# Performance work log

Hardware: AMD Instinct MI355X
Metric: run time of the kernel (lower is better)

Reference implementation:

```python
import jax, jax.numpy as jnp
import numpy as np
from jax import lax

V, H, A, S = 256, 2048, 512, 512  # vocab, hidden, attn, seq_len


def setup_inputs() -> dict:
    key = jax.random.key(0)
    ks = jax.random.split(key, 8)
    sc = 0.02  # small init to keep tanh unsaturated
    return {
        "x_enc": jax.random.normal(ks[0], (S, V), jnp.float32),
        "x_dec": jax.random.normal(ks[1], (S, V), jnp.float32),
        "W_enc": jax.random.normal(ks[2], (H, V + H), jnp.float32) * sc,
        "b_enc": jnp.zeros((H,), jnp.float32),
        "Wa_enc": jax.random.normal(ks[3], (A, H), jnp.float32) * sc,
        "Wa_dec": jax.random.normal(ks[4], (A, H), jnp.float32) * sc,
        "v_a": jax.random.normal(ks[5], (A,), jnp.float32) * sc,
        "W_dec": jax.random.normal(ks[6], (H, V + 2 * H), jnp.float32) * sc,
        "b_dec": jnp.zeros((H,), jnp.float32),
        "W_out": jax.random.normal(ks[7], (V, H), jnp.float32) * sc,
        "b_out": jnp.zeros((V,), jnp.float32),
    }


def reference(x_enc, x_dec, W_enc, b_enc, Wa_enc, Wa_dec, v_a, W_dec, b_dec, W_out, b_out):
    h0 = jnp.zeros((W_enc.shape[0],), x_enc.dtype)

    # Encoder: h_t = tanh(W_enc [x_t ; h_{t-1}] + b)
    def enc_step(h, x):
        h_new = jnp.tanh(jnp.concatenate([x, h]) @ W_enc.T + b_enc)
        return h_new, h_new

    h_enc, enc_states = lax.scan(enc_step, h0, x_enc)  # enc_states: (S, H)

    # Encoder-side attention projection is step-invariant -> hoist (same math).
    enc_proj = enc_states @ Wa_enc.T  # (S, A)

    # Decoder with per-step Bahdanau additive attention.
    def dec_step(h, x):
        dec_proj = h @ Wa_dec.T                              # (A,)
        energy = jnp.tanh(enc_proj + dec_proj) @ v_a         # (S,)
        attn_w = jax.nn.softmax(energy)                      # (S,)
        context = attn_w @ enc_states                        # (H,)
        h_new = jnp.tanh(jnp.concatenate([x, context, h]) @ W_dec.T + b_dec)
        logits = h_new @ W_out.T + b_out                     # (V,)
        return h_new, logits

    _, outputs = lax.scan(dec_step, h_enc, x_dec)  # (S, V)
    return outputs
```

## Files before the change

### kernel.cpp

```cpp
#include <hip/hip_runtime.h>

#define V 256
#define H 2048
#define A 512
#define S 512
#define NBLK 128
#define NTHR 512
#define CH 64

typedef float f32x4 __attribute__((ext_vector_type(4)));

__device__ __forceinline__ void st_chunk(float* p, float x, float y, int tag) {
    f32x4 v; v.x = x; v.y = y; v.z = 0.f; v.w = __int_as_float(tag);
    asm volatile("global_store_dwordx4 %0, %1, off sc0 sc1" :: "v"(p), "v"(v) : "memory");
}
__device__ __forceinline__ f32x4 poll1(const float* p, int tag) {
    f32x4 r;
    for (;;) {
        asm volatile("global_load_dwordx4 %0, %1, off sc0 sc1\n\ts_waitcnt vmcnt(0)"
                     : "=&v"(r) : "v"(p) : "memory");
        if (__float_as_int(r.w) == tag) return r;
    }
}
__device__ __forceinline__ void poll2(const float* p0, const float* p1, int tag,
                                      f32x4& a, f32x4& b) {
    for (;;) {
        asm volatile("global_load_dwordx4 %0, %2, off sc0 sc1\n\t"
                     "global_load_dwordx4 %1, %3, off sc0 sc1\n\t"
                     "s_waitcnt vmcnt(0)"
                     : "=&v"(a), "=&v"(b) : "v"(p0), "v"(p1) : "memory");
        if (__float_as_int(a.w) == tag && __float_as_int(b.w) == tag) return;
    }
}

__global__ void init_ex(float* p, int n) {
    int i = blockIdx.x * blockDim.x + threadIdx.x;
    if (i < n) p[i] = 0.f;
}

__global__ __launch_bounds__(256) void gemm_nt(
    const float* __restrict__ Amat, int lda,
    const float* __restrict__ Bmat, int ldb,
    float* __restrict__ C, int ldc,
    const float* __restrict__ bias, int M, int N, int K)
{
    __shared__ float As[16][68];
    __shared__ float Bs[16][68];
    const int tid = threadIdx.x;
    const int tx = tid & 15;
    const int ty = tid >> 4;
    const int m0 = blockIdx.y * 64;
    const int n0 = blockIdx.x * 64;
    const int lr = tid >> 2;
    const int lk = (tid & 3) * 4;

    float acc[4][4] = {};
    for (int k0 = 0; k0 < K; k0 += 16) {
        float4 av = *(const float4*)(Amat + (size_t)(m0 + lr) * lda + k0 + lk);
        float4 bv = *(const float4*)(Bmat + (size_t)(n0 + lr) * ldb + k0 + lk);
        __syncthreads();
        As[lk+0][lr] = av.x; As[lk+1][lr] = av.y; As[lk+2][lr] = av.z; As[lk+3][lr] = av.w;
        Bs[lk+0][lr] = bv.x; Bs[lk+1][lr] = bv.y; Bs[lk+2][lr] = bv.z; Bs[lk+3][lr] = bv.w;
        __syncthreads();
        #pragma unroll
        for (int k = 0; k < 16; ++k) {
            float a4[4], b4[4];
            #pragma unroll
            for (int i = 0; i < 4; ++i) a4[i] = As[k][ty*4+i];
            #pragma unroll
            for (int j = 0; j < 4; ++j) b4[j] = Bs[k][tx*4+j];
            #pragma unroll
            for (int i = 0; i < 4; ++i)
                #pragma unroll
                for (int j = 0; j < 4; ++j) acc[i][j] += a4[i] * b4[j];
        }
    }
    #pragma unroll
    for (int i = 0; i < 4; ++i) {
        const int m = m0 + ty*4 + i;
        #pragma unroll
        for (int j = 0; j < 4; ++j) {
            const int n = n0 + tx*4 + j;
            float v = acc[i][j];
            if (bias) v += bias[n];
            C[(size_t)m * ldc + n] = v;
        }
    }
}

__global__ __launch_bounds__(NTHR, 2) void enc_scan(
    const float* __restrict__ W_enc, const float* __restrict__ accx,
    float* __restrict__ states, float* __restrict__ hex)
{
    __shared__ __align__(16) float hs[2][H];
    const int tid = threadIdx.x;
    const int wid = tid >> 6, lane = tid & 63;
    const int w   = blockIdx.x * 8 + wid;
    const int r0  = 2*w, r1 = r0 + 1;

    f32x4 we0[8], we1[8];
    #pragma unroll
    for (int k = 0; k < 8; ++k) {
        we0[k] = *(const f32x4*)(W_enc + (size_t)r0*(V+H) + V + 4*(lane + 64*k));
        we1[k] = *(const f32x4*)(W_enc + (size_t)r1*(V+H) + V + 4*(lane + 64*k));
    }

    if (lane == 0) {
        float h0 = tanhf(accx[r0]), h1 = tanhf(accx[r1]);
        states[r0] = h0; states[r1] = h1;
        st_chunk(hex + w*CH, h0, h1, 1);
    }

    for (int t = 1; t < S; ++t) {
        float ax0 = 0.f, ax1 = 0.f;
        if (lane == 0) {
            ax0 = accx[(size_t)t*H + r0];
            ax1 = accx[(size_t)t*H + r1];
        }
        f32x4 ca, cb;
        const float* hb = hex + ((t-1)&1)*(1024*CH);
        poll2(hb + (2*tid)*CH, hb + (2*tid+1)*CH, t, ca, cb);
        float* dst = hs[t&1];
        dst[4*tid+0] = ca.x; dst[4*tid+1] = ca.y;
        dst[4*tid+2] = cb.x; dst[4*tid+3] = cb.y;
        __syncthreads();

        const f32x4* h4 = (const f32x4*)hs[t&1];
        float a0 = 0.f, a1 = 0.f;
        #pragma unroll
        for (int k = 0; k < 8; ++k) {
            f32x4 hv = h4[lane + 64*k];
            a0 += we0[k].x*hv.x + we0[k].y*hv.y + we0[k].z*hv.z + we0[k].w*hv.w;
            a1 += we1[k].x*hv.x + we1[k].y*hv.y + we1[k].z*hv.z + we1[k].w*hv.w;
        }
        #pragma unroll
        for (int off = 32; off; off >>= 1) { a0 += __shfl_down(a0, off); a1 += __shfl_down(a1, off); }
        if (lane == 0) {
            float h0 = tanhf(a0 + ax0);
            float h1 = tanhf(a1 + ax1);
            states[(size_t)t*H + r0] = h0; states[(size_t)t*H + r1] = h1;
            st_chunk(hex + (t&1)*(1024*CH) + w*CH, h0, h1, t+1);
        }
    }
}

__global__ __launch_bounds__(NTHR, 2) void dec_scan(
    const float* __restrict__ Wa_dec, const float* __restrict__ W_dec,
    const float* __restrict__ enc_proj, const float* __restrict__ v_a,
    const float* __restrict__ WcT, const float* __restrict__ accx,
    const float* __restrict__ enc_states, float* __restrict__ h_dec,
    float* __restrict__ hexd, float* __restrict__ dpex, float* __restrict__ eex)
{
    __shared__ __align__(16) float hs[H];
    __shared__ __align__(16) float ps[A];
    __shared__ __align__(16) float es[S];
    __shared__ float zred[8];
    const int tid = threadIdx.x;
    const int wid = tid >> 6, lane = tid & 63;
    const int w   = blockIdx.x * 8 + wid;
    const int r0  = 2*w, r1 = r0 + 1;
    const bool attn_blk = (blockIdx.x < 64);

    f32x4 wh0[8], wh1[8], wa[8], wc0[2], wc1[2], ep[2], va[2];
    #pragma unroll
    for (int k = 0; k < 8; ++k) {
        wh0[k] = *(const f32x4*)(W_dec + (size_t)r0*(V+2*H) + V + H + 4*(lane + 64*k));
        wh1[k] = *(const f32x4*)(W_dec + (size_t)r1*(V+2*H) + V + H + 4*(lane + 64*k));
        wa[k]  = (f32x4)(0.f);
    }
    #pragma unroll
    for (int k = 0; k < 2; ++k) {
        wc0[k] = *(const f32x4*)(WcT + (size_t)r0*S + 4*(lane + 64*k));
        wc1[k] = *(const f32x4*)(WcT + (size_t)r1*S + 4*(lane + 64*k));
        ep[k] = (f32x4)(0.f); va[k] = (f32x4)(0.f);
    }
    if (attn_blk) {
        #pragma unroll
        for (int k = 0; k < 8; ++k)
            wa[k] = *(const f32x4*)(Wa_dec + (size_t)w*H + 4*(lane + 64*k));
        #pragma unroll
        for (int k = 0; k < 2; ++k) {
            ep[k] = *(const f32x4*)(enc_proj + (size_t)w*A + 4*(lane + 64*k));
            va[k] = *(const f32x4*)(v_a + 4*(lane + 64*k));
        }
    }
    const f32x4* hs4 = (const f32x4*)hs;
    const f32x4* ps4 = (const f32x4*)ps;
    const f32x4* es4 = (const f32x4*)es;

    for (int t = 0; t < S; ++t) {
        float ax0 = 0.f, ax1 = 0.f;
        if (lane == 0) {
            ax0 = accx[(size_t)t*H + r0];
            ax1 = accx[(size_t)t*H + r1];
        }

        if (t == 0) {
            ((f32x4*)hs)[tid] = ((const f32x4*)(enc_states + (size_t)(S-1)*H))[tid];
        } else {
            f32x4 ca, cb;
            const float* hb = hexd + ((t-1)&1)*(1024*CH);
            poll2(hb + (2*tid)*CH, hb + (2*tid+1)*CH, t, ca, cb);
            hs[4*tid+0] = ca.x; hs[4*tid+1] = ca.y;
            hs[4*tid+2] = cb.x; hs[4*tid+3] = cb.y;
        }
        __syncthreads();

        if (attn_blk) {
            float aP = 0.f;
            #pragma unroll
            for (int k = 0; k < 8; ++k) {
                f32x4 hv = hs4[lane + 64*k];
                aP += wa[k].x*hv.x + wa[k].y*hv.y + wa[k].z*hv.z + wa[k].w*hv.w;
            }
            #pragma unroll
            for (int off = 32; off; off >>= 1) aP += __shfl_down(aP, off);
            if (lane == 0) st_chunk(dpex + (t&1)*(512*CH) + w*CH, aP, 0.f, t+1);
        }
        float aH0 = 0.f, aH1 = 0.f;
        #pragma unroll
        for (int k = 0; k < 8; ++k) {
            f32x4 hv = hs4[lane + 64*k];
            aH0 += wh0[k].x*hv.x + wh0[k].y*hv.y + wh0[k].z*hv.z + wh0[k].w*hv.w;
            aH1 += wh1[k].x*hv.x + wh1[k].y*hv.y + wh1[k].z*hv.z + wh1[k].w*hv.w;
        }
        #pragma unroll
        for (int off = 32; off; off >>= 1) { aH0 += __shfl_down(aH0, off); aH1 += __shfl_down(aH1, off); }

        if (attn_blk) {
            f32x4 c = poll1(dpex + (t&1)*(512*CH) + tid*CH, t+1);
            ps[tid] = c.x;
            __syncthreads();
            float e_ = 0.f;
            #pragma unroll
            for (int k = 0; k < 2; ++k) {
                f32x4 p = ps4[lane + 64*k];
                e_ += va[k].x*tanhf(ep[k].x + p.x) + va[k].y*tanhf(ep[k].y + p.y)
                    + va[k].z*tanhf(ep[k].z + p.z) + va[k].w*tanhf(ep[k].w + p.w);
            }
            #pragma unroll
            for (int off = 32; off; off >>= 1) e_ += __shfl_down(e_, off);
            if (lane == 0) st_chunk(eex + (t&1)*(512*CH) + w*CH, expf(e_), 0.f, t+1);
        }

        {
            f32x4 c = poll1(eex + (t&1)*(512*CH) + tid*CH, t+1);
            es[tid] = c.x;
        }
        __syncthreads();

        float z = es[tid];
        #pragma unroll
        for (int off = 32; off; off >>= 1) z += __shfl_down(z, off);
        if (lane == 0) zred[wid] = z;
        __syncthreads();
        const float Z = zred[0]+zred[1]+zred[2]+zred[3]+zred[4]+zred[5]+zred[6]+zred[7];

        float c0 = 0.f, c1 = 0.f;
        #pragma unroll
        for (int k = 0; k < 2; ++k) {
            f32x4 ev = es4[lane + 64*k];
            c0 += wc0[k].x*ev.x + wc0[k].y*ev.y + wc0[k].z*ev.z + wc0[k].w*ev.w;
            c1 += wc1[k].x*ev.x + wc1[k].y*ev.y + wc1[k].z*ev.z + wc1[k].w*ev.w;
        }
        #pragma unroll
        for (int off = 32; off; off >>= 1) { c0 += __shfl_down(c0, off); c1 += __shfl_down(c1, off); }
        if (lane == 0) {
            const float Zi = 1.f / Z;
            float h0 = tanhf(ax0 + aH0 + c0*Zi);
            float h1 = tanhf(ax1 + aH1 + c1*Zi);
            h_dec[(size_t)t*H + r0] = h0; h_dec[(size_t)t*H + r1] = h1;
            st_chunk(hexd + (t&1)*(1024*CH) + w*CH, h0, h1, t+1);
        }
    }
}

extern "C" void kernel_launch(void* const* d_in, const int* in_sizes, int n_in,
                              void* d_out, int out_size, void* d_ws, size_t ws_size,
                              hipStream_t stream) {
    const float* x_enc  = (const float*)d_in[0];
    const float* x_dec  = (const float*)d_in[1];
    const float* W_enc  = (const float*)d_in[2];
    const float* b_enc  = (const float*)d_in[3];
    const float* Wa_enc = (const float*)d_in[4];
    const float* Wa_dec = (const float*)d_in[5];
    const float* v_a    = (const float*)d_in[6];
    const float* W_dec  = (const float*)d_in[7];
    const float* b_dec  = (const float*)d_in[8];
    const float* W_out  = (const float*)d_in[9];
    const float* b_out  = (const float*)d_in[10];
    float* out = (float*)d_out;

    float* ws         = (float*)d_ws;
    float* accx_enc   = ws;
    float* enc_states = accx_enc + (size_t)S*H;
    float* enc_proj   = enc_states + (size_t)S*H;
    float* WcT        = enc_proj + (size_t)S*A;
    float* accx_dec   = WcT + (size_t)H*S;
    float* h_dec      = accx_dec + (size_t)S*H;
    float* hex_e      = h_dec + (size_t)S*H;
    float* hex_d      = hex_e + 2*1024*CH;
    float* dp_ex      = hex_d + 2*1024*CH;
    float* e_ex       = dp_ex + 2*512*CH;
    const int n_ex = 2*1024*CH + 2*1024*CH + 2*512*CH + 2*512*CH;

    dim3 b256(256);

    init_ex<<<dim3((n_ex + 255)/256), b256, 0, stream>>>(hex_e, n_ex);

    gemm_nt<<<dim3(H/64, S/64), b256, 0, stream>>>(x_enc, V, W_enc, V+H, accx_enc, H, b_enc, S, H, V);
    gemm_nt<<<dim3(H/64, S/64), b256, 0, stream>>>(x_dec, V, W_dec, V+2*H, accx_dec, H, b_dec, S, H, V);

    {
        const float* We = W_enc; const float* ax = accx_enc; float* st = enc_states; float* hx = hex_e;
        void* args[] = { &We, &ax, &st, &hx };
        hipLaunchCooperativeKernel((void*)enc_scan, dim3(NBLK), dim3(NTHR), args, 0, stream);
    }

    gemm_nt<<<dim3(A/64, S/64), b256, 0, stream>>>(enc_states, H, Wa_enc, H, enc_proj, A, nullptr, S, A, H);
    gemm_nt<<<dim3(S/64, H/64), b256, 0, stream>>>(W_dec + V, V+2*H, enc_states, H, WcT, S, nullptr, H, S, H);

    {
        const float* wa = Wa_dec; const float* wd = W_dec; const float* epj = enc_proj;
        const float* vv = v_a; const float* wc = WcT; const float* ax = accx_dec;
        const float* est = enc_states; float* hd = h_dec;
        float* hx = hex_d; float* dx = dp_ex; float* ex = e_ex;
        void* args[] = { &wa, &wd, &epj, &vv, &wc, &ax, &est, &hd, &hx, &dx, &ex };
        hipLaunchCooperativeKernel((void*)dec_scan, dim3(NBLK), dim3(NTHR), args, 0, stream);
    }

    gemm_nt<<<dim3(V/64, S/64), b256, 0, stream>>>(h_dec, H, W_out, H, out, V, b_out, S, V, H);
}
```

Baseline: 6.103 ms.

## Halve persistent grid to 64 blocks with four rows per wave

Both persistent scan kernels now run on 64 blocks instead of 128. Each wave owns four hidden rows, keeps 4x8 weight vectors in registers, and writes two exchange chunks per step. In the decoder every block now takes part in attention, with enc_proj and v_a staged in shared memory. Polling loops gain an s_sleep backoff to cut memory traffic while spinning. The goal is fewer participants in the grid-wide spin barrier, but each wave does twice the dot-product work per step and register pressure grows.

```diff
diff --git a/kernel.cpp b/kernel.cpp
--- a/kernel.cpp
+++ b/kernel.cpp
@@ -4,7 +4,7 @@
 #define H 2048
 #define A 512
 #define S 512
-#define NBLK 128
+#define NBLK 64
 #define NTHR 512
 #define CH 64
 
@@ -14,22 +14,26 @@
     f32x4 v; v.x = x; v.y = y; v.z = 0.f; v.w = __int_as_float(tag);
     asm volatile("global_store_dwordx4 %0, %1, off sc0 sc1" :: "v"(p), "v"(v) : "memory");
 }
+__device__ __forceinline__ f32x4 ld_cg4(const float* p) {
+    f32x4 r;
+    asm volatile("global_load_dwordx4 %0, %1, off sc0 sc1\n\ts_waitcnt vmcnt(0)"
+                 : "=&v"(r) : "v"(p) : "memory");
+    return r;
+}
 __device__ __forceinline__ f32x4 poll1(const float* p, int tag) {
-    f32x4 r;
-    for (;;) {
-        asm volatile("global_load_dwordx4 %0, %1, off sc0 sc1\n\ts_waitcnt vmcnt(0)"
-                     : "=&v"(r) : "v"(p) : "memory");
-        if (__float_as_int(r.w) == tag) return r;
-    }
+    f32x4 r = ld_cg4(p);
+    while (__float_as_int(r.w) != tag) {
+        __builtin_amdgcn_s_sleep(2);
+        r = ld_cg4(p);
+    }
+    return r;
 }
 __device__ __forceinline__ void poll2(const float* p0, const float* p1, int tag,
                                       f32x4& a, f32x4& b) {
-    for (;;) {
-        asm volatile("global_load_dwordx4 %0, %2, off sc0 sc1\n\t"
-                     "global_load_dwordx4 %1, %3, off sc0 sc1\n\t"
-                     "s_waitcnt vmcnt(0)"
-                     : "=&v"(a), "=&v"(b) : "v"(p0), "v"(p1) : "memory");
-        if (__float_as_int(a.w) == tag && __float_as_int(b.w) == tag) return;
+    a = ld_cg4(p0); b = ld_cg4(p1);
+    while (__float_as_int(a.w) != tag || __float_as_int(b.w) != tag) {
+        __builtin_amdgcn_s_sleep(2);
+        a = ld_cg4(p0); b = ld_cg4(p1);
     }
 }
 
@@ -88,7 +92,7 @@
     }
 }
 
-__global__ __launch_bounds__(NTHR, 2) void enc_scan(
+__global__ __launch_bounds__(NTHR, 1) void enc_scan(
     const float* __restrict__ W_enc, const float* __restrict__ accx,
     float* __restrict__ states, float* __restrict__ hex)
 {
@@ -96,27 +100,27 @@
     const int tid = threadIdx.x;
     const int wid = tid >> 6, lane = tid & 63;
     const int w   = blockIdx.x * 8 + wid;
-    const int r0  = 2*w, r1 = r0 + 1;
-
-    f32x4 we0[8], we1[8];
-    #pragma unroll
-    for (int k = 0; k < 8; ++k) {
-        we0[k] = *(const f32x4*)(W_enc + (size_t)r0*(V+H) + V + 4*(lane + 64*k));
-        we1[k] = *(const f32x4*)(W_enc + (size_t)r1*(V+H) + V + 4*(lane + 64*k));
-    }
+    const int r0  = 4*w;
+
+    f32x4 we[4][8];
+    #pragma unroll
+    for (int r = 0; r < 4; ++r)
+        #pragma unroll
+        for (int k = 0; k < 8; ++k)
+            we[r][k] = *(const f32x4*)(W_enc + (size_t)(r0+r)*(V+H) + V + 4*(lane + 64*k));
 
     if (lane == 0) {
-        float h0 = tanhf(accx[r0]), h1 = tanhf(accx[r1]);
-        states[r0] = h0; states[r1] = h1;
-        st_chunk(hex + w*CH, h0, h1, 1);
+        f32x4 ax = *(const f32x4*)(accx + r0);
+        float h0 = tanhf(ax.x), h1 = tanhf(ax.y), h2 = tanhf(ax.z), h3 = tanhf(ax.w);
+        f32x4 hv; hv.x = h0; hv.y = h1; hv.z = h2; hv.w = h3;
+        *(f32x4*)(states + r0) = hv;
+        st_chunk(hex + (2*w)*CH,   h0, h1, 1);
+        st_chunk(hex + (2*w+1)*CH, h2, h3, 1);
     }
 
     for (int t = 1; t < S; ++t) {
-        float ax0 = 0.f, ax1 = 0.f;
-        if (lane == 0) {
-            ax0 = accx[(size_t)t*H + r0];
-            ax1 = accx[(size_t)t*H + r1];
-        }
+        f32x4 ax;
+        if (lane == 0) ax = *(const f32x4*)(accx + (size_t)t*H + r0);
         f32x4 ca, cb;
         const float* hb = hex + ((t-1)&1)*(1024*CH);
         poll2(hb + (2*tid)*CH, hb + (2*tid+1)*CH, t, ca, cb);
@@ -126,25 +130,33 @@
         __syncthreads();
 
         const f32x4* h4 = (const f32x4*)hs[t&1];
-        float a0 = 0.f, a1 = 0.f;
+        float a0 = 0.f, a1 = 0.f, a2 = 0.f, a3 = 0.f;
         #pragma unroll
         for (int k = 0; k < 8; ++k) {
             f32x4 hv = h4[lane + 64*k];
-            a0 += we0[k].x*hv.x + we0[k].y*hv.y + we0[k].z*hv.z + we0[k].w*hv.w;
-            a1 += we1[k].x*hv.x + we1[k].y*hv.y + we1[k].z*hv.z + we1[k].w*hv.w;
-        }
-        #pragma unroll
-        for (int off = 32; off; off >>= 1) { a0 += __shfl_down(a0, off); a1 += __shfl_down(a1, off); }
+            a0 += we[0][k].x*hv.x + we[0][k].y*hv.y + we[0][k].z*hv.z + we[0][k].w*hv.w;
+            a1 += we[1][k].x*hv.x + we[1][k].y*hv.y + we[1][k].z*hv.z + we[1][k].w*hv.w;
+            a2 += we[2][k].x*hv.x + we[2][k].y*hv.y + we[2][k].z*hv.z + we[2][k].w*hv.w;
+            a3 += we[3][k].x*hv.x + we[3][k].y*hv.y + we[3][k].z*hv.z + we[3][k].w*hv.w;
+        }
+        #pragma unroll
+        for (int off = 32; off; off >>= 1) {
+            a0 += __shfl_down(a0, off); a1 += __shfl_down(a1, off);
+            a2 += __shfl_down(a2, off); a3 += __shfl_down(a3, off);
+        }
         if (lane == 0) {
-            float h0 = tanhf(a0 + ax0);
-            float h1 = tanhf(a1 + ax1);
-            states[(size_t)t*H + r0] = h0; states[(size_t)t*H + r1] = h1;
-            st_chunk(hex + (t&1)*(1024*CH) + w*CH, h0, h1, t+1);
-        }
-    }
-}
-
-__global__ __launch_bounds__(NTHR, 2) void dec_scan(
+            float h0 = tanhf(a0 + ax.x), h1 = tanhf(a1 + ax.y);
+            float h2 = tanhf(a2 + ax.z), h3 = tanhf(a3 + ax.w);
+            f32x4 hv; hv.x = h0; hv.y = h1; hv.z = h2; hv.w = h3;
+            *(f32x4*)(states + (size_t)t*H + r0) = hv;
+            float* ob = hex + (t&1)*(1024*CH);
+            st_chunk(ob + (2*w)*CH,   h0, h1, t+1);
+            st_chunk(ob + (2*w+1)*CH, h2, h3, t+1);
+        }
+    }
+}
+
+__global__ __launch_bounds__(NTHR, 1) void dec_scan(
     const float* __restrict__ Wa_dec, const float* __restrict__ W_dec,
     const float* __restrict__ enc_proj, const float* __restrict__ v_a,
     const float* __restrict__ WcT, const float* __restrict__ accx,
@@ -154,46 +166,42 @@
     __shared__ __align__(16) float hs[H];
     __shared__ __align__(16) float ps[A];
     __shared__ __align__(16) float es[S];
+    __shared__ __align__(16) float va[A];
+    __shared__ __align__(16) float epl[8][A];
     __shared__ float zred[8];
     const int tid = threadIdx.x;
     const int wid = tid >> 6, lane = tid & 63;
     const int w   = blockIdx.x * 8 + wid;
-    const int r0  = 2*w, r1 = r0 + 1;
-    const bool attn_blk = (blockIdx.x < 64);
-
-    f32x4 wh0[8], wh1[8], wa[8], wc0[2], wc1[2], ep[2], va[2];
-    #pragma unroll
-    for (int k = 0; k < 8; ++k) {
-        wh0[k] = *(const f32x4*)(W_dec + (size_t)r0*(V+2*H) + V + H + 4*(lane + 64*k));
-        wh1[k] = *(const f32x4*)(W_dec + (size_t)r1*(V+2*H) + V + H + 4*(lane + 64*k));
-        wa[k]  = (f32x4)(0.f);
-    }
-    #pragma unroll
-    for (int k = 0; k < 2; ++k) {
-        wc0[k] = *(const f32x4*)(WcT + (size_t)r0*S + 4*(lane + 64*k));
-        wc1[k] = *(const f32x4*)(WcT + (size_t)r1*S + 4*(lane + 64*k));
-        ep[k] = (f32x4)(0.f); va[k] = (f32x4)(0.f);
-    }
-    if (attn_blk) {
+    const int r0  = 4*w;
+
+    f32x4 wh[4][8], wa[8], wc[4][2];
+    #pragma unroll
+    for (int r = 0; r < 4; ++r)
         #pragma unroll
         for (int k = 0; k < 8; ++k)
-            wa[k] = *(const f32x4*)(Wa_dec + (size_t)w*H + 4*(lane + 64*k));
-        #pragma unroll
-        for (int k = 0; k < 2; ++k) {
-            ep[k] = *(const f32x4*)(enc_proj + (size_t)w*A + 4*(lane + 64*k));
-            va[k] = *(const f32x4*)(v_a + 4*(lane + 64*k));
-        }
-    }
+            wh[r][k] = *(const f32x4*)(W_dec + (size_t)(r0+r)*(V+2*H) + V + H + 4*(lane + 64*k));
+    #pragma unroll
+    for (int k = 0; k < 8; ++k)
+        wa[k] = *(const f32x4*)(Wa_dec + (size_t)w*H + 4*(lane + 64*k));
+    #pragma unroll
+    for (int r = 0; r < 4; ++r)
+        #pragma unroll
+        for (int k = 0; k < 2; ++k)
+            wc[r][k] = *(const f32x4*)(WcT + (size_t)(r0+r)*S + 4*(lane + 64*k));
+
+    if (tid < A/4) ((f32x4*)va)[tid] = *(const f32x4*)(v_a + 4*tid);
+    #pragma unroll
+    for (int k = 0; k < 2; ++k)
+        *(f32x4*)(&epl[wid][4*(lane + 64*k)]) =
+            *(const f32x4*)(enc_proj + (size_t)w*A + 4*(lane + 64*k));
+
     const f32x4* hs4 = (const f32x4*)hs;
     const f32x4* ps4 = (const f32x4*)ps;
     const f32x4* es4 = (const f32x4*)es;
 
     for (int t = 0; t < S; ++t) {
-        float ax0 = 0.f, ax1 = 0.f;
-        if (lane == 0) {
-            ax0 = accx[(size_t)t*H + r0];
-            ax1 = accx[(size_t)t*H + r1];
-        }
+        f32x4 ax;
+        if (lane == 0) ax = *(const f32x4*)(accx + (size_t)t*H + r0);
 
         if (t == 0) {
             ((f32x4*)hs)[tid] = ((const f32x4*)(enc_states + (size_t)(S-1)*H))[tid];
@@ -206,7 +214,7 @@
         }
         __syncthreads();
 
-        if (attn_blk) {
+        {
             float aP = 0.f;
             #pragma unroll
             for (int k = 0; k < 8; ++k) {
@@ -217,26 +225,35 @@
             for (int off = 32; off; off >>= 1) aP += __shfl_down(aP, off);
             if (lane == 0) st_chunk(dpex + (t&1)*(512*CH) + w*CH, aP, 0.f, t+1);
         }
-        float aH0 = 0.f, aH1 = 0.f;
+        float aH0 = 0.f, aH1 = 0.f, aH2 = 0.f, aH3 = 0.f;
         #pragma unroll
         for (int k = 0; k < 8; ++k) {
             f32x4 hv = hs4[lane + 64*k];
-            aH0 += wh0[k].x*hv.x + wh0[k].y*hv.y + wh0[k].z*hv.z + wh0[k].w*hv.w;
-            aH1 += wh1[k].x*hv.x + wh1[k].y*hv.y + wh1[k].z*hv.z + wh1[k].w*hv.w;
-        }
-        #pragma unroll
-        for (int off = 32; off; off >>= 1) { aH0 += __shfl_down(aH0, off); aH1 += __shfl_down(aH1, off); }
-
-        if (attn_blk) {
+            aH0 += wh[0][k].x*hv.x + wh[0][k].y*hv.y + wh[0][k].z*hv.z + wh[0][k].w*hv.w;
+            aH1 += wh[1][k].x*hv.x + wh[1][k].y*hv.y + wh[1][k].z*hv.z + wh[1][k].w*hv.w;
+            aH2 += wh[2][k].x*hv.x + wh[2][k].y*hv.y + wh[2][k].z*hv.z + wh[2][k].w*hv.w;
+            aH3 += wh[3][k].x*hv.x + wh[3][k].y*hv.y + wh[3][k].z*hv.z + wh[3][k].w*hv.w;
+        }
+        #pragma unroll
+        for (int off = 32; off; off >>= 1) {
+            aH0 += __shfl_down(aH0, off); aH1 += __shfl_down(aH1, off);
+            aH2 += __shfl_down(aH2, off); aH3 += __shfl_down(aH3, off);
+        }
+
+        {
             f32x4 c = poll1(dpex + (t&1)*(512*CH) + tid*CH, t+1);
             ps[tid] = c.x;
-            __syncthreads();
+        }
+        __syncthreads();
+        {
             float e_ = 0.f;
             #pragma unroll
             for (int k = 0; k < 2; ++k) {
-                f32x4 p = ps4[lane + 64*k];
-                e_ += va[k].x*tanhf(ep[k].x + p.x) + va[k].y*tanhf(ep[k].y + p.y)
-                    + va[k].z*tanhf(ep[k].z + p.z) + va[k].w*tanhf(ep[k].w + p.w);
+                f32x4 p  = ps4[lane + 64*k];
+                f32x4 e4 = *(const f32x4*)(&epl[wid][4*(lane + 64*k)]);
+                f32x4 v4 = *(const f32x4*)(&va[4*(lane + 64*k)]);
+                e_ += v4.x*tanhf(e4.x + p.x) + v4.y*tanhf(e4.y + p.y)
+                    + v4.z*tanhf(e4.z + p.z) + v4.w*tanhf(e4.w + p.w);
             }
             #pragma unroll
             for (int off = 32; off; off >>= 1) e_ += __shfl_down(e_, off);
@@ -256,21 +273,31 @@
         __syncthreads();
         const float Z = zred[0]+zred[1]+zred[2]+zred[3]+zred[4]+zred[5]+zred[6]+zred[7];
 
-        float c0 = 0.f, c1 = 0.f;
+        float c0 = 0.f, c1 = 0.f, c2 = 0.f, c3 = 0.f;
         #pragma unroll
         for (int k = 0; k < 2; ++k) {
             f32x4 ev = es4[lane + 64*k];
-            c0 += wc0[k].x*ev.x + wc0[k].y*ev.y + wc0[k].z*ev.z + wc0[k].w*ev.w;
-            c1 += wc1[k].x*ev.x + wc1[k].y*ev.y + wc1[k].z*ev.z + wc1[k].w*ev.w;
-        }
-        #pragma unroll
-        for (int off = 32; off; off >>= 1) { c0 += __shfl_down(c0, off); c1 += __shfl_down(c1, off); }
+            c0 += wc[0][k].x*ev.x + wc[0][k].y*ev.y + wc[0][k].z*ev.z + wc[0][k].w*ev.w;
+            c1 += wc[1][k].x*ev.x + wc[1][k].y*ev.y + wc[1][k].z*ev.z + wc[1][k].w*ev.w;
+            c2 += wc[2][k].x*ev.x + wc[2][k].y*ev.y + wc[2][k].z*ev.z + wc[2][k].w*ev.w;
+            c3 += wc[3][k].x*ev.x + wc[3][k].y*ev.y + wc[3][k].z*ev.z + wc[3][k].w*ev.w;
+        }
+        #pragma unroll
+        for (int off = 32; off; off >>= 1) {
+            c0 += __shfl_down(c0, off); c1 += __shfl_down(c1, off);
+            c2 += __shfl_down(c2, off); c3 += __shfl_down(c3, off);
+        }
         if (lane == 0) {
             const float Zi = 1.f / Z;
-            float h0 = tanhf(ax0 + aH0 + c0*Zi);
-            float h1 = tanhf(ax1 + aH1 + c1*Zi);
-            h_dec[(size_t)t*H + r0] = h0; h_dec[(size_t)t*H + r1] = h1;
-            st_chunk(hexd + (t&1)*(1024*CH) + w*CH, h0, h1, t+1);
+            float h0 = tanhf(ax.x + aH0 + c0*Zi);
+            float h1 = tanhf(ax.y + aH1 + c1*Zi);
+            float h2 = tanhf(ax.z + aH2 + c2*Zi);
+            float h3 = tanhf(ax.w + aH3 + c3*Zi);
+            f32x4 hv; hv.x = h0; hv.y = h1; hv.z = h2; hv.w = h3;
+            *(f32x4*)(h_dec + (size_t)t*H + r0) = hv;
+            float* ob = hexd + (t&1)*(1024*CH);
+            st_chunk(ob + (2*w)*CH,   h0, h1, t+1);
+            st_chunk(ob + (2*w+1)*CH, h2, h3, t+1);
         }
     }
 }
```

New measurement: 7.668 ms. +25.6%, slower.

## Pack exchange values densely and use NaN-sentinel triple buffering for cross-block sync

Applied to the files above, without the earlier changes.

Replaces per-value tagged 16-byte chunks with densely packed exchange slots, four values per 16-byte line, that start out holding a NaN sentinel. Readers spin until no lane holds the sentinel, and each writer resets its slot two steps ahead in a three-deep ring. This halves or quarters the number of polling loads per thread per step, and in the decoder the attention work is spread across interleaved warps in every block. The risk is that correctness relies on ordering of the reset and publish stores and on real results never equalling the sentinel bit pattern.

```diff
diff --git a/kernel.cpp b/kernel.cpp
--- a/kernel.cpp
+++ b/kernel.cpp
@@ -7,35 +7,47 @@
 #define NBLK 128
 #define NTHR 512
 #define CH 64
+#define HPH (512*CH)
+#define DPH (128*CH)
+#define SENTU 0x7FC00000u
 
 typedef float f32x4 __attribute__((ext_vector_type(4)));
-
-__device__ __forceinline__ void st_chunk(float* p, float x, float y, int tag) {
-    f32x4 v; v.x = x; v.y = y; v.z = 0.f; v.w = __int_as_float(tag);
-    asm volatile("global_store_dwordx4 %0, %1, off sc0 sc1" :: "v"(p), "v"(v) : "memory");
-}
-__device__ __forceinline__ f32x4 poll1(const float* p, int tag) {
+typedef float f32x2 __attribute__((ext_vector_type(2)));
+
+__device__ __forceinline__ f32x4 ld_cg4(const float* p) {
     f32x4 r;
-    for (;;) {
-        asm volatile("global_load_dwordx4 %0, %1, off sc0 sc1\n\ts_waitcnt vmcnt(0)"
-                     : "=&v"(r) : "v"(p) : "memory");
-        if (__float_as_int(r.w) == tag) return r;
-    }
-}
-__device__ __forceinline__ void poll2(const float* p0, const float* p1, int tag,
-                                      f32x4& a, f32x4& b) {
-    for (;;) {
-        asm volatile("global_load_dwordx4 %0, %2, off sc0 sc1\n\t"
-                     "global_load_dwordx4 %1, %3, off sc0 sc1\n\t"
-                     "s_waitcnt vmcnt(0)"
-                     : "=&v"(a), "=&v"(b) : "v"(p0), "v"(p1) : "memory");
-        if (__float_as_int(a.w) == tag && __float_as_int(b.w) == tag) return;
-    }
-}
-
-__global__ void init_ex(float* p, int n) {
+    asm volatile("global_load_dwordx4 %0, %1, off sc0 sc1\n\ts_waitcnt vmcnt(0)"
+                 : "=&v"(r) : "v"(p) : "memory");
+    return r;
+}
+__device__ __forceinline__ f32x4 poll4(const float* p) {
+    f32x4 r = ld_cg4(p);
+    while (__float_as_uint(r.x) == SENTU || __float_as_uint(r.y) == SENTU ||
+           __float_as_uint(r.z) == SENTU || __float_as_uint(r.w) == SENTU)
+        r = ld_cg4(p);
+    return r;
+}
+__device__ __forceinline__ void st_pub2(float* p, float x, float y) {
+    f32x2 v; v.x = x; v.y = y;
+    asm volatile("s_waitcnt vmcnt(0)\n\tglobal_store_dwordx2 %0, %1, off sc0 sc1"
+                 :: "v"(p), "v"(v) : "memory");
+}
+__device__ __forceinline__ void st_pub1(float* p, float x) {
+    asm volatile("s_waitcnt vmcnt(0)\n\tglobal_store_dword %0, %1, off sc0 sc1"
+                 :: "v"(p), "v"(x) : "memory");
+}
+__device__ __forceinline__ void st_rst2(float* p) {
+    f32x2 v; v.x = __uint_as_float(SENTU); v.y = __uint_as_float(SENTU);
+    asm volatile("global_store_dwordx2 %0, %1, off sc0 sc1" :: "v"(p), "v"(v) : "memory");
+}
+__device__ __forceinline__ void st_rst1(float* p) {
+    float v = __uint_as_float(SENTU);
+    asm volatile("global_store_dword %0, %1, off sc0 sc1" :: "v"(p), "v"(v) : "memory");
+}
+
+__global__ void init_ex(unsigned* p, int n) {
     int i = blockIdx.x * blockDim.x + threadIdx.x;
-    if (i < n) p[i] = 0.f;
+    if (i < n) p[i] = SENTU;
 }
 
 __global__ __launch_bounds__(256) void gemm_nt(
@@ -97,6 +109,7 @@
     const int wid = tid >> 6, lane = tid & 63;
     const int w   = blockIdx.x * 8 + wid;
     const int r0  = 2*w, r1 = r0 + 1;
+    const int slot = (w >> 1)*CH + (w & 1)*2;
 
     f32x4 we0[8], we1[8];
     #pragma unroll
@@ -108,22 +121,18 @@
     if (lane == 0) {
         float h0 = tanhf(accx[r0]), h1 = tanhf(accx[r1]);
         states[r0] = h0; states[r1] = h1;
-        st_chunk(hex + w*CH, h0, h1, 1);
+        st_pub2(hex + slot, h0, h1);
     }
 
     for (int t = 1; t < S; ++t) {
         float ax0 = 0.f, ax1 = 0.f;
-        if (lane == 0) {
-            ax0 = accx[(size_t)t*H + r0];
-            ax1 = accx[(size_t)t*H + r1];
-        }
-        f32x4 ca, cb;
-        const float* hb = hex + ((t-1)&1)*(1024*CH);
-        poll2(hb + (2*tid)*CH, hb + (2*tid+1)*CH, t, ca, cb);
-        float* dst = hs[t&1];
-        dst[4*tid+0] = ca.x; dst[4*tid+1] = ca.y;
-        dst[4*tid+2] = cb.x; dst[4*tid+3] = cb.y;
-        __syncthreads();
+        if (lane == 0) { ax0 = accx[(size_t)t*H + r0]; ax1 = accx[(size_t)t*H + r1]; }
+
+        f32x4 c = poll4(hex + ((t-1)%3)*HPH + tid*CH);
+        ((f32x4*)hs[t&1])[tid] = c;
+        __syncthreads();
+
+        if (lane == 0) st_rst2(hex + ((t+1)%3)*HPH + slot);
 
         const f32x4* h4 = (const f32x4*)hs[t&1];
         float a0 = 0.f, a1 = 0.f;
@@ -139,7 +148,7 @@
             float h0 = tanhf(a0 + ax0);
             float h1 = tanhf(a1 + ax1);
             states[(size_t)t*H + r0] = h0; states[(size_t)t*H + r1] = h1;
-            st_chunk(hex + (t&1)*(1024*CH) + w*CH, h0, h1, t+1);
+            st_pub2(hex + (t%3)*HPH + slot, h0, h1);
         }
     }
 }
@@ -159,7 +168,10 @@
     const int wid = tid >> 6, lane = tid & 63;
     const int w   = blockIdx.x * 8 + wid;
     const int r0  = 2*w, r1 = r0 + 1;
-    const bool attn_blk = (blockIdx.x < 64);
+    const int hslot = (w >> 1)*CH + (w & 1)*2;
+    const bool attn = ((w & 1) == 0);
+    const int s_row = w >> 1;
+    const int aslot = (s_row >> 2)*CH + (s_row & 3);
 
     f32x4 wh0[8], wh1[8], wa[8], wc0[2], wc1[2], ep[2], va[2];
     #pragma unroll
@@ -174,13 +186,13 @@
         wc1[k] = *(const f32x4*)(WcT + (size_t)r1*S + 4*(lane + 64*k));
         ep[k] = (f32x4)(0.f); va[k] = (f32x4)(0.f);
     }
-    if (attn_blk) {
+    if (attn) {
         #pragma unroll
         for (int k = 0; k < 8; ++k)
-            wa[k] = *(const f32x4*)(Wa_dec + (size_t)w*H + 4*(lane + 64*k));
+            wa[k] = *(const f32x4*)(Wa_dec + (size_t)s_row*H + 4*(lane + 64*k));
         #pragma unroll
         for (int k = 0; k < 2; ++k) {
-            ep[k] = *(const f32x4*)(enc_proj + (size_t)w*A + 4*(lane + 64*k));
+            ep[k] = *(const f32x4*)(enc_proj + (size_t)s_row*A + 4*(lane + 64*k));
             va[k] = *(const f32x4*)(v_a + 4*(lane + 64*k));
         }
     }
@@ -190,23 +202,25 @@
 
     for (int t = 0; t < S; ++t) {
         float ax0 = 0.f, ax1 = 0.f;
-        if (lane == 0) {
-            ax0 = accx[(size_t)t*H + r0];
-            ax1 = accx[(size_t)t*H + r1];
-        }
+        if (lane == 0) { ax0 = accx[(size_t)t*H + r0]; ax1 = accx[(size_t)t*H + r1]; }
 
         if (t == 0) {
             ((f32x4*)hs)[tid] = ((const f32x4*)(enc_states + (size_t)(S-1)*H))[tid];
         } else {
-            f32x4 ca, cb;
-            const float* hb = hexd + ((t-1)&1)*(1024*CH);
-            poll2(hb + (2*tid)*CH, hb + (2*tid+1)*CH, t, ca, cb);
-            hs[4*tid+0] = ca.x; hs[4*tid+1] = ca.y;
-            hs[4*tid+2] = cb.x; hs[4*tid+3] = cb.y;
-        }
-        __syncthreads();
-
-        if (attn_blk) {
+            f32x4 c = poll4(hexd + ((t-1)%3)*HPH + tid*CH);
+            ((f32x4*)hs)[tid] = c;
+        }
+        __syncthreads();
+
+        if (t > 0 && lane == 0) {
+            st_rst2(hexd + ((t+1)%3)*HPH + hslot);
+            if (attn) {
+                st_rst1(dpex + ((t-1)%3)*DPH + aslot);
+                st_rst1(eex  + ((t-1)%3)*DPH + aslot);
+            }
+        }
+
+        if (attn) {
             float aP = 0.f;
             #pragma unroll
             for (int k = 0; k < 8; ++k) {
@@ -215,7 +229,7 @@
             }
             #pragma unroll
             for (int off = 32; off; off >>= 1) aP += __shfl_down(aP, off);
-            if (lane == 0) st_chunk(dpex + (t&1)*(512*CH) + w*CH, aP, 0.f, t+1);
+            if (lane == 0) st_pub1(dpex + (t%3)*DPH + aslot, aP);
         }
         float aH0 = 0.f, aH1 = 0.f;
         #pragma unroll
@@ -227,10 +241,12 @@
         #pragma unroll
         for (int off = 32; off; off >>= 1) { aH0 += __shfl_down(aH0, off); aH1 += __shfl_down(aH1, off); }
 
-        if (attn_blk) {
-            f32x4 c = poll1(dpex + (t&1)*(512*CH) + tid*CH, t+1);
-            ps[tid] = c.x;
-            __syncthreads();
+        if (tid < 128) {
+            f32x4 c = poll4(dpex + (t%3)*DPH + tid*CH);
+            ((f32x4*)ps)[tid] = c;
+        }
+        __syncthreads();
+        if (attn) {
             float e_ = 0.f;
             #pragma unroll
             for (int k = 0; k < 2; ++k) {
@@ -240,12 +256,12 @@
             }
             #pragma unroll
             for (int off = 32; off; off >>= 1) e_ += __shfl_down(e_, off);
-            if (lane == 0) st_chunk(eex + (t&1)*(512*CH) + w*CH, expf(e_), 0.f, t+1);
-        }
-
-        {
-            f32x4 c = poll1(eex + (t&1)*(512*CH) + tid*CH, t+1);
-            es[tid] = c.x;
+            if (lane == 0) st_pub1(eex + (t%3)*DPH + aslot, expf(e_));
+        }
+
+        if (tid < 128) {
+            f32x4 c = poll4(eex + (t%3)*DPH + tid*CH);
+            ((f32x4*)es)[tid] = c;
         }
         __syncthreads();
 
@@ -270,7 +286,7 @@
             float h0 = tanhf(ax0 + aH0 + c0*Zi);
             float h1 = tanhf(ax1 + aH1 + c1*Zi);
             h_dec[(size_t)t*H + r0] = h0; h_dec[(size_t)t*H + r1] = h1;
-            st_chunk(hexd + (t&1)*(1024*CH) + w*CH, h0, h1, t+1);
+            st_pub2(hexd + (t%3)*HPH + hslot, h0, h1);
         }
     }
 }
@@ -299,14 +315,14 @@
     float* accx_dec   = WcT + (size_t)H*S;
     float* h_dec      = accx_dec + (size_t)S*H;
     float* hex_e      = h_dec + (size_t)S*H;
-    float* hex_d      = hex_e + 2*1024*CH;
-    float* dp_ex      = hex_d + 2*1024*CH;
-    float* e_ex       = dp_ex + 2*512*CH;
-    const int n_ex = 2*1024*CH + 2*1024*CH + 2*512*CH + 2*512*CH;
+    float* hex_d      = hex_e + 3*HPH;
+    float* dp_ex      = hex_d + 3*HPH;
+    float* e_ex       = dp_ex + 3*DPH;
+    const int n_ex = 3*HPH*2 + 3*DPH*2;
 
     dim3 b256(256);
 
-    init_ex<<<dim3((n_ex + 255)/256), b256, 0, stream>>>(hex_e, n_ex);
+    init_ex<<<dim3((n_ex + 255)/256), b256, 0, stream>>>((unsigned*)hex_e, n_ex);
 
     gemm_nt<<<dim3(H/64, S/64), b256, 0, stream>>>(x_enc, V, W_enc, V+H, accx_enc, H, b_enc, S, H, V);
     gemm_nt<<<dim3(H/64, S/64), b256, 0, stream>>>(x_dec, V, W_dec, V+2*H, accx_dec, H, b_dec, S, H, V);
```

Measured after the change: 6.185 ms. Within noise of the previous version (+1.3%).
